# Performance work log

Hardware: AMD Instinct MI355X
Metric: run time of the kernel (lower is better)

## Reference

```python
import jax, jax.numpy as jnp
import numpy as np


def _log_g(x):
    # numerically stable log of g(x) = where(x>=0, x+0.5, sigmoid(x))
    return jnp.where(x >= 0, jnp.log(jax.nn.relu(x) + 0.5), -jax.nn.softplus(-x))


def setup_inputs() -> dict:
    key = jax.random.key(0)
    k1, k2, k3, k4 = jax.random.split(key, 4)
    B, T, D = 4, 4096, 1024
    Di = 2 * D  # dim_inner = int(dim * expansion_factor), expansion_factor = 2.0
    x = jax.random.normal(k1, (B, T, D), dtype=jnp.float32)
    prev_hidden = jax.random.uniform(k2, (B, Di), dtype=jnp.float32)  # positive carry state
    # torch Linear(dim, 2*dim_inner, bias=False): stored here pre-transposed as [D, 2*Di]
    W_hg = jax.random.normal(k3, (D, 2 * Di), dtype=jnp.float32) * (1.0 / np.sqrt(D))
    # out_proj Linear(dim_inner, dim, bias=False): stored pre-transposed as [Di, D]
    W_out = jax.random.normal(k4, (Di, D), dtype=jnp.float32) * (1.0 / np.sqrt(Di))
    return {"x": x, "prev_hidden": prev_hidden, "W_hg": W_hg, "W_out": W_out}


def reference(x, prev_hidden, W_hg, W_out):
    # x: [B, T, D]; prev_hidden: [B, Di] (positive)
    T = x.shape[1]
    hg = jnp.einsum('btd,de->bte', x, W_hg)          # [B, T, 2*Di]
    hidden, gate = jnp.split(hg, 2, axis=-1)          # each [B, T, Di]

    # Heinsen log-space affine scan: h_t = (1 - z_t) * h_{t-1} + z_t * g(hidden_t)
    log_coeffs = -jax.nn.softplus(gate)               # log(1 - sigmoid(gate))
    log_values = -jax.nn.softplus(-gate) + _log_g(hidden)  # log(sigmoid(gate)) + log g(hidden)

    # prepend carry state
    prev_log = jnp.clip(jnp.log(jnp.clip(prev_hidden, 1e-8, None)), -30.0, None)[:, None]  # [B,1,Di]
    log_values = jnp.concatenate([prev_log, log_values], axis=1)      # [B, T+1, Di]
    log_coeffs = jnp.pad(log_coeffs, ((0, 0), (1, 0), (0, 0)))        # [B, T+1, Di]

    a_star = jnp.cumsum(log_coeffs, axis=1)
    h = jnp.exp(a_star + jax.lax.cumlogsumexp(log_values - a_star, axis=1))  # [B, T+1, Di]
    h = h[:, -T:]                                     # drop carry slot

    next_hidden = h[:, -1]                            # [B, Di]
    out = jnp.einsum('bte,ed->btd', h, W_out)         # [B, T, D]
    return (out, next_hidden)
```

## Files before the change

kernel.cpp:

```cpp
#include <hip/hip_runtime.h>
#include <cstdio>

#define T_LEN 4096
#define B_SZ  4
#define D_IN  1024
#define DI    2048
#define MM    16384
#define NC2   64
#define CHL2  64

typedef __attribute__((ext_vector_type(8))) __bf16 bf16x8;
typedef __attribute__((ext_vector_type(4))) float  f32x4;
typedef __attribute__((ext_vector_type(8))) unsigned short u16x8;

__device__ __forceinline__ unsigned short f2bf(float f){
  unsigned u = __builtin_bit_cast(unsigned, f);
  u += 0x7fffu + ((u >> 16) & 1u);
  return (unsigned short)(u >> 16);
}
__device__ __forceinline__ float bf2f_lo(unsigned u){
  return __builtin_bit_cast(float, u << 16);
}
__device__ __forceinline__ float bf2f_hi(unsigned u){
  return __builtin_bit_cast(float, u & 0xffff0000u);
}

__device__ __forceinline__ void async16(void* lds, const void* g){
  __builtin_amdgcn_global_load_lds((const __attribute__((address_space(1))) void*)g,
                                   (__attribute__((address_space(3))) void*)lds, 16, 0, 0);
}

template<int PERM>
__device__ __forceinline__ void transpose_body(const float* __restrict__ src,
                                               unsigned short* __restrict__ dst,
                                               int n0, int k0, int SK, int SN,
                                               float (*tile)[65], int tid){
  #pragma unroll
  for(int it=0; it<16; it++){
    int idx = it*256 + tid;
    int kk = idx>>6, nn = idx&63;
    int n = n0+nn;
    int col = PERM ? (((n>>5)<<4) + (n&15) + ((n&16)?2048:0)) : n;
    tile[kk][nn] = src[(size_t)(k0+kk)*SN + col];
  }
  __syncthreads();
  #pragma unroll
  for(int it=0; it<16; it++){
    int idx = it*256 + tid;
    int nn = idx>>6, kk = idx&63;
    dst[(size_t)(n0+nn)*SK + k0+kk] = f2bf(tile[kk][nn]);
  }
}

__global__ __launch_bounds__(256) void k_prep(const float* __restrict__ x,
                                              unsigned short* __restrict__ xb,
                                              const float* __restrict__ Whg,
                                              unsigned short* __restrict__ wt,
                                              const float* __restrict__ Wout,
                                              unsigned short* __restrict__ wo){
  __shared__ float tile[64][65];
  int bid = blockIdx.x, tid = threadIdx.x;
  if(bid < 8192){
    size_t t = (size_t)bid*256 + tid;
    const float4* xi = (const float4*)x;
    float4 a = xi[2*t], b = xi[2*t+1];
    u16x8 o;
    o[0]=f2bf(a.x); o[1]=f2bf(a.y); o[2]=f2bf(a.z); o[3]=f2bf(a.w);
    o[4]=f2bf(b.x); o[5]=f2bf(b.y); o[6]=f2bf(b.z); o[7]=f2bf(b.w);
    ((u16x8*)xb)[t] = o;
  } else if(bid < 9216){
    int j = bid - 8192;
    transpose_body<1>(Whg, wt, (j&63)*64, (j>>6)*64, 1024, 4096, tile, tid);
  } else {
    int j = bid - 9216;
    transpose_body<0>(Wout, wo, (j&15)*64, (j>>4)*64, 2048, 1024, tile, tid);
  }
}

template<int EPI>
__global__ __launch_bounds__(256, 2)
void k_gemm(const unsigned short* __restrict__ A, const unsigned short* __restrict__ Bt,
            float* __restrict__ C0, unsigned short* __restrict__ U0,
            unsigned short* __restrict__ U1, float* __restrict__ Ap,
            float* __restrict__ Vp, int M, int N, int K){
  __shared__ unsigned short lsA[128*32];
  __shared__ unsigned short lsB[128*32];
  int tid  = threadIdx.x;
  int lane = tid & 63, wave = tid >> 6;
  int wm = wave >> 1, wn = wave & 1;
  int cl = lane & 15, quad = lane >> 4;
  int m0 = blockIdx.y * 128, n0 = blockIdx.x * 128;

  f32x4 acc[4][4];
  #pragma unroll
  for(int i=0;i<4;i++)
    #pragma unroll
    for(int j=0;j<4;j++) acc[i][j] = (f32x4){0.f,0.f,0.f,0.f};

  int cs = (tid&3) ^ ((tid>>3)&3);
  const unsigned short* gA = A  + (size_t)(m0 + (tid>>2))*K + cs*8;
  const unsigned short* gB = Bt + (size_t)(n0 + (tid>>2))*K + cs*8;
  unsigned short* dA = lsA + tid*8;
  unsigned short* dB = lsB + tid*8;
  int qa8 = (quad ^ ((cl>>1)&3)) * 8;

  for(int k0=0; k0<K; k0+=32){
    async16(dA,        gA + k0);
    async16(dA + 2048, gA + (size_t)64*K + k0);
    async16(dB,        gB + k0);
    async16(dB + 2048, gB + (size_t)64*K + k0);
    __syncthreads();
    bf16x8 fa[4], fb[4];
    #pragma unroll
    for(int t2=0;t2<4;t2++){
      fa[t2] = *(const bf16x8*)&lsA[(wm*64 + t2*16 + cl)*32 + qa8];
      fb[t2] = *(const bf16x8*)&lsB[(wn*64 + t2*16 + cl)*32 + qa8];
    }
    #pragma unroll
    for(int i=0;i<4;i++)
      #pragma unroll
      for(int j=0;j<4;j++)
        acc[i][j] = __builtin_amdgcn_mfma_f32_16x16x32_bf16(fa[i], fb[j], acc[i][j], 0, 0, 0);
    __syncthreads();
  }

  if(EPI==0){
    #pragma unroll
    for(int i=0;i<4;i++)
      #pragma unroll
      for(int j=0;j<4;j++){
        int n = n0 + wn*64 + j*16 + cl;
        #pragma unroll
        for(int r=0;r<4;r++){
          int m = m0 + wm*64 + i*16 + quad*4 + r;
          C0[(size_t)m*N + n] = acc[i][j][r];
        }
      }
  } else {
    float* lA_f = (float*)lsA;
    float* lV_f = (float*)lsB;
    int ibase = ((n0 + wn*64) >> 1) + cl;
    #pragma unroll
    for(int i=0;i<4;i++)
      #pragma unroll
      for(int p=0;p<2;p++){
        f32x4 hh = acc[i][2*p], gg = acc[i][2*p+1];
        int ii = ibase + p*16;
        float pa = 1.f, pv = 0.f;
        #pragma unroll
        for(int r=0;r<4;r++){
          int m = m0 + wm*64 + i*16 + quad*4 + r;
          float gate = gg[r], hid = hh[r];
          float e  = __expf(gate);
          float cc = 1.f/(1.f + e);
          float z  = (gate > 80.f) ? 1.f : e*cc;
          float gv = (hid >= 0.f) ? (hid + 0.5f) : (1.f/(1.f + __expf(-hid)));
          float vv = z*gv;
          U0[(size_t)m*DI + ii] = f2bf(cc);
          U1[(size_t)m*DI + ii] = f2bf(vv);
          pa *= cc;
          pv = fmaf(cc, pv, vv);
        }
        int seg = wm*16 + i*4 + quad;
        int chl = wn*32 + p*16 + cl;
        lA_f[seg*64 + chl] = pa;
        lV_f[seg*64 + chl] = pv;
      }
    __syncthreads();
    if(tid < 128){
      int ch = tid & 63, q = tid >> 6;
      float Ac = 1.f, Vc = 0.f;
      #pragma unroll 8
      for(int s=0; s<16; s++){
        int idx = (q*16 + s)*64 + ch;
        float a = lA_f[idx], v = lV_f[idx];
        Ac *= a;
        Vc = fmaf(a, Vc, v);
      }
      int b = m0 >> 12;
      int ch64 = ((m0 & 4095) >> 6) + q;
      size_t o = (size_t)(b*NC2 + ch64)*DI + (n0 >> 1) + ch;
      Ap[o] = Ac; Vp[o] = Vc;
    }
  }
}

__global__ __launch_bounds__(256) void k_scanB(const float* __restrict__ prev,
                                               float* __restrict__ Ap,
                                               const float* __restrict__ Vp){
  int t = blockIdx.x*256 + threadIdx.x;
  int i = t & (DI-1); int b = t >> 11;
  float h = fmaxf(prev[t], 1e-8f);
  for(int ch=0; ch<NC2; ch++){
    size_t o = (size_t)(b*NC2 + ch)*DI + i;
    float a = Ap[o], vv = Vp[o];
    Ap[o] = h;
    h = fmaf(a, h, vv);
  }
}

__global__ __launch_bounds__(256) void k_scanC(const unsigned* __restrict__ cp,
                                               unsigned* __restrict__ vp,
                                               const float* __restrict__ hin,
                                               float* __restrict__ nh){
  int t = blockIdx.x*256 + threadIdx.x;
  int i2 = t & (DI/2 - 1);
  int ch = (t >> 10) & (NC2-1);
  int b  = t >> 16;
  size_t base = ((size_t)(b*T_LEN + ch*CHL2))*(DI/2) + i2;
  const float2* hin2 = (const float2*)hin;
  float2 h01 = hin2[(size_t)(b*NC2 + ch)*(DI/2) + i2];
  float h0 = h01.x, h1 = h01.y;
  #pragma unroll 4
  for(int s=0; s<CHL2; s++){
    unsigned cu = cp[base], vu = vp[base];
    h0 = fmaf(bf2f_lo(cu), h0, bf2f_lo(vu));
    h1 = fmaf(bf2f_hi(cu), h1, bf2f_hi(vu));
    vp[base] = (unsigned)f2bf(h0) | ((unsigned)f2bf(h1) << 16);
    base += DI/2;
  }
  if(ch == NC2-1){ nh[b*DI + 2*i2] = h0; nh[b*DI + 2*i2 + 1] = h1; }
}

extern "C" void kernel_launch(void* const* d_in, const int* in_sizes, int n_in,
                              void* d_out, int out_size, void* d_ws, size_t ws_size,
                              hipStream_t stream){
  const float* x    = (const float*)d_in[0];
  const float* prev = (const float*)d_in[1];
  const float* Whg  = (const float*)d_in[2];
  const float* Wout = (const float*)d_in[3];
  float* out = (float*)d_out;
  float* nh  = out + (size_t)MM*D_IN;

  const size_t NEED = 117440512;
  if(ws_size < NEED){
    fprintf(stderr, "kernel_launch: ws_size=%zu < needed %zu — aborting launch\n",
            ws_size, NEED);
    return;
  }
  char* ws = (char*)d_ws;
  unsigned short* xb = (unsigned short*)(ws);
  unsigned short* wt = (unsigned short*)(ws + 33554432);
  unsigned short* wo = (unsigned short*)(ws + 41943040);
  unsigned short* v  = (unsigned short*)(ws + 46137344);
  float* Ap  = (float*)(ws + 113246208);
  float* Vp  = (float*)(ws + 115343360);
  unsigned short* c = (unsigned short*)d_out;

  k_prep<<<9728, 256, 0, stream>>>(x, xb, Whg, wt, Wout, wo);

  k_gemm<1><<<dim3(32,128), 256, 0, stream>>>(xb, wt, nullptr, c, v, Ap, Vp,
                                              MM, 2*DI, D_IN);

  k_scanB<<<32,   256, 0, stream>>>(prev, Ap, Vp);
  k_scanC<<<1024, 256, 0, stream>>>((const unsigned*)c, (unsigned*)v, Ap, nh);

  k_gemm<0><<<dim3(8,128), 256, 0, stream>>>(v, wo, out, nullptr, nullptr,
                                             nullptr, nullptr, MM, D_IN, DI);
}
```

Baseline: 424.6 us.

## Deepen GEMM K-tile, pack bf16 stores, halve scan chunks with bf16 carries

The GEMM now stages a 64-wide K slice per iteration with an 8-way XOR swizzle, which halves the number of barrier pairs per tile. The epilogue uses lane shuffles so each lane writes one packed 32-bit word instead of two scattered 16-bit stores. The chunked scan uses 128 chunks of 32 steps instead of 64 of 64, so the per-chunk pass runs with more parallel threads. Chunk carries are stored as bf16 to cut traffic, at the cost of carry precision and a longer serial carry pass over 128 chunks.

```diff
diff --git a/kernel.cpp b/kernel.cpp
--- a/kernel.cpp
+++ b/kernel.cpp
@@ -6,8 +6,8 @@
 #define D_IN  1024
 #define DI    2048
 #define MM    16384
-#define NC2   64
-#define CHL2  64
+#define NC2   128
+#define CHL2  32
 
 typedef __attribute__((ext_vector_type(8))) __bf16 bf16x8;
 typedef __attribute__((ext_vector_type(4))) float  f32x4;
@@ -23,6 +23,9 @@
 }
 __device__ __forceinline__ float bf2f_hi(unsigned u){
   return __builtin_bit_cast(float, u & 0xffff0000u);
+}
+__device__ __forceinline__ float bf2f_s(unsigned short s){
+  return __builtin_bit_cast(float, (unsigned)s << 16);
 }
 
 __device__ __forceinline__ void async16(void* lds, const void* g){
@@ -80,11 +83,11 @@
 template<int EPI>
 __global__ __launch_bounds__(256, 2)
 void k_gemm(const unsigned short* __restrict__ A, const unsigned short* __restrict__ Bt,
-            float* __restrict__ C0, unsigned short* __restrict__ U0,
-            unsigned short* __restrict__ U1, float* __restrict__ Ap,
-            float* __restrict__ Vp, int M, int N, int K){
-  __shared__ unsigned short lsA[128*32];
-  __shared__ unsigned short lsB[128*32];
+            float* __restrict__ C0, unsigned* __restrict__ U0,
+            unsigned* __restrict__ U1, unsigned short* __restrict__ Ap,
+            unsigned short* __restrict__ Vp, int M, int N, int K){
+  __shared__ unsigned short lsA[128*64];
+  __shared__ unsigned short lsB[128*64];
   int tid  = threadIdx.x;
   int lane = tid & 63, wave = tid >> 6;
   int wm = wave >> 1, wn = wave & 1;
@@ -97,30 +100,36 @@
     #pragma unroll
     for(int j=0;j<4;j++) acc[i][j] = (f32x4){0.f,0.f,0.f,0.f};
 
-  int cs = (tid&3) ^ ((tid>>3)&3);
-  const unsigned short* gA = A  + (size_t)(m0 + (tid>>2))*K + cs*8;
-  const unsigned short* gB = Bt + (size_t)(n0 + (tid>>2))*K + cs*8;
+  int g = (tid&7) ^ ((tid>>3)&7);
+  const unsigned short* gA = A  + (size_t)(m0 + (tid>>3))*K + g*8;
+  const unsigned short* gB = Bt + (size_t)(n0 + (tid>>3))*K + g*8;
   unsigned short* dA = lsA + tid*8;
   unsigned short* dB = lsB + tid*8;
-  int qa8 = (quad ^ ((cl>>1)&3)) * 8;
-
-  for(int k0=0; k0<K; k0+=32){
-    async16(dA,        gA + k0);
-    async16(dA + 2048, gA + (size_t)64*K + k0);
-    async16(dB,        gB + k0);
-    async16(dB + 2048, gB + (size_t)64*K + k0);
+
+  for(int k0=0; k0<K; k0+=64){
+    #pragma unroll
+    for(int it=0; it<4; it++){
+      async16(dA + it*2048, gA + (size_t)(it*32)*K + k0);
+      async16(dB + it*2048, gB + (size_t)(it*32)*K + k0);
+    }
     __syncthreads();
-    bf16x8 fa[4], fb[4];
-    #pragma unroll
-    for(int t2=0;t2<4;t2++){
-      fa[t2] = *(const bf16x8*)&lsA[(wm*64 + t2*16 + cl)*32 + qa8];
-      fb[t2] = *(const bf16x8*)&lsB[(wn*64 + t2*16 + cl)*32 + qa8];
+    #pragma unroll
+    for(int kh=0; kh<2; kh++){
+      bf16x8 fa[4], fb[4];
+      int sl = ((kh<<2)|quad);
+      #pragma unroll
+      for(int t2=0;t2<4;t2++){
+        int ra = wm*64 + t2*16 + cl;
+        int rb = wn*64 + t2*16 + cl;
+        fa[t2] = *(const bf16x8*)&lsA[ra*64 + (sl^(cl&7))*8];
+        fb[t2] = *(const bf16x8*)&lsB[rb*64 + (sl^(cl&7))*8];
+      }
+      #pragma unroll
+      for(int i=0;i<4;i++)
+        #pragma unroll
+        for(int j=0;j<4;j++)
+          acc[i][j] = __builtin_amdgcn_mfma_f32_16x16x32_bf16(fa[i], fb[j], acc[i][j], 0, 0, 0);
     }
-    #pragma unroll
-    for(int i=0;i<4;i++)
-      #pragma unroll
-      for(int j=0;j<4;j++)
-        acc[i][j] = __builtin_amdgcn_mfma_f32_16x16x32_bf16(fa[i], fb[j], acc[i][j], 0, 0, 0);
     __syncthreads();
   }
 
@@ -140,6 +149,7 @@
     float* lA_f = (float*)lsA;
     float* lV_f = (float*)lsB;
     int ibase = ((n0 + wn*64) >> 1) + cl;
+    int odd = cl & 1;
     #pragma unroll
     for(int i=0;i<4;i++)
       #pragma unroll
@@ -156,8 +166,12 @@
           float z  = (gate > 80.f) ? 1.f : e*cc;
           float gv = (hid >= 0.f) ? (hid + 0.5f) : (1.f/(1.f + __expf(-hid)));
           float vv = z*gv;
-          U0[(size_t)m*DI + ii] = f2bf(cc);
-          U1[(size_t)m*DI + ii] = f2bf(vv);
+          float ccp = __shfl_xor(cc, 1, 64);
+          float vvp = __shfl_xor(vv, 1, 64);
+          unsigned wlo = odd ? (unsigned)f2bf(vvp) : (unsigned)f2bf(cc);
+          unsigned whi = odd ? (unsigned)f2bf(vv)  : (unsigned)f2bf(ccp);
+          unsigned* dst = odd ? U1 : U0;
+          dst[((size_t)m*DI + (ii & ~1)) >> 1] = wlo | (whi << 16);
           pa *= cc;
           pv = fmaf(cc, pv, vv);
         }
@@ -167,50 +181,49 @@
         lV_f[seg*64 + chl] = pv;
       }
     __syncthreads();
-    if(tid < 128){
+    {
       int ch = tid & 63, q = tid >> 6;
       float Ac = 1.f, Vc = 0.f;
-      #pragma unroll 8
-      for(int s=0; s<16; s++){
-        int idx = (q*16 + s)*64 + ch;
+      #pragma unroll
+      for(int s=0; s<8; s++){
+        int idx = (q*8 + s)*64 + ch;
         float a = lA_f[idx], v = lV_f[idx];
         Ac *= a;
         Vc = fmaf(a, Vc, v);
       }
       int b = m0 >> 12;
-      int ch64 = ((m0 & 4095) >> 6) + q;
-      size_t o = (size_t)(b*NC2 + ch64)*DI + (n0 >> 1) + ch;
-      Ap[o] = Ac; Vp[o] = Vc;
+      int ch32 = ((m0 & 4095) >> 5) + q;
+      size_t o = (size_t)(b*NC2 + ch32)*DI + (n0 >> 1) + ch;
+      Ap[o] = f2bf(Ac); Vp[o] = f2bf(Vc);
     }
   }
 }
 
 __global__ __launch_bounds__(256) void k_scanB(const float* __restrict__ prev,
-                                               float* __restrict__ Ap,
-                                               const float* __restrict__ Vp){
+                                               unsigned short* __restrict__ Ap,
+                                               const unsigned short* __restrict__ Vp){
   int t = blockIdx.x*256 + threadIdx.x;
   int i = t & (DI-1); int b = t >> 11;
   float h = fmaxf(prev[t], 1e-8f);
   for(int ch=0; ch<NC2; ch++){
     size_t o = (size_t)(b*NC2 + ch)*DI + i;
-    float a = Ap[o], vv = Vp[o];
-    Ap[o] = h;
+    float a = bf2f_s(Ap[o]), vv = bf2f_s(Vp[o]);
+    Ap[o] = f2bf(h);
     h = fmaf(a, h, vv);
   }
 }
 
 __global__ __launch_bounds__(256) void k_scanC(const unsigned* __restrict__ cp,
                                                unsigned* __restrict__ vp,
-                                               const float* __restrict__ hin,
+                                               const unsigned* __restrict__ hinp,
                                                float* __restrict__ nh){
   int t = blockIdx.x*256 + threadIdx.x;
   int i2 = t & (DI/2 - 1);
   int ch = (t >> 10) & (NC2-1);
-  int b  = t >> 16;
+  int b  = t >> 17;
   size_t base = ((size_t)(b*T_LEN + ch*CHL2))*(DI/2) + i2;
-  const float2* hin2 = (const float2*)hin;
-  float2 h01 = hin2[(size_t)(b*NC2 + ch)*(DI/2) + i2];
-  float h0 = h01.x, h1 = h01.y;
+  unsigned hp = hinp[(size_t)(b*NC2 + ch)*(DI/2) + i2];
+  float h0 = bf2f_lo(hp), h1 = bf2f_hi(hp);
   #pragma unroll 4
   for(int s=0; s<CHL2; s++){
     unsigned cu = cp[base], vu = vp[base];
@@ -243,17 +256,18 @@
   unsigned short* wt = (unsigned short*)(ws + 33554432);
   unsigned short* wo = (unsigned short*)(ws + 41943040);
   unsigned short* v  = (unsigned short*)(ws + 46137344);
-  float* Ap  = (float*)(ws + 113246208);
-  float* Vp  = (float*)(ws + 115343360);
-  unsigned short* c = (unsigned short*)d_out;
+  unsigned short* Ap = (unsigned short*)(ws + 113246208);
+  unsigned short* Vp = (unsigned short*)(ws + 115343360);
+  unsigned* c = (unsigned*)d_out;
 
   k_prep<<<9728, 256, 0, stream>>>(x, xb, Whg, wt, Wout, wo);
 
-  k_gemm<1><<<dim3(32,128), 256, 0, stream>>>(xb, wt, nullptr, c, v, Ap, Vp,
-                                              MM, 2*DI, D_IN);
+  k_gemm<1><<<dim3(32,128), 256, 0, stream>>>(xb, wt, nullptr, c, (unsigned*)v,
+                                              Ap, Vp, MM, 2*DI, D_IN);
 
   k_scanB<<<32,   256, 0, stream>>>(prev, Ap, Vp);
-  k_scanC<<<1024, 256, 0, stream>>>((const unsigned*)c, (unsigned*)v, Ap, nh);
+  k_scanC<<<2048, 256, 0, stream>>>((const unsigned*)c, (unsigned*)v,
+                                    (const unsigned*)Ap, nh);
 
   k_gemm<0><<<dim3(8,128), 256, 0, stream>>>(v, wo, out, nullptr, nullptr,
                                              nullptr, nullptr, MM, D_IN, DI);
```

Measured after the change: 421.7 us. About the same (-0.7%).
